# Optimization experiments

Hardware: AMD Instinct MI355X
Metric: run time of the kernel (lower is better)

## Reference

```python
import jax, jax.numpy as jnp
import numpy as np

B, T, V, EMB, H, SRC, NSRC = 128, 128, 50000, 1024, 512, 100, 3
D = EMB + 2 * H + SRC          # 2148, actual concat dim (cim* executable path)
HALF = D // 2                  # 1074
NUM_LABELS = 2


def setup_inputs() -> dict:
    key = jax.random.key(0)
    ks = jax.random.split(key, 32)
    s = 0.05
    n = lambda k, shp: jax.random.normal(k, shp, dtype=jnp.float32) * s
    inp = {
        "article": jax.random.randint(ks[0], (B, T), 0, V),
        "positions": jax.random.randint(ks[1], (B,), 0, T),
        "srcs": jax.random.randint(ks[2], (B,), 0, NSRC),
        "E": jax.random.normal(ks[3], (V, EMB), dtype=jnp.float32),
        "src_emb": n(ks[4], (NSRC, SRC)),
        # BiLSTM layer 0 (input EMB), forward / backward direction cells
        "Wih0f": n(ks[5], (4 * H, EMB)), "Whh0f": n(ks[6], (4 * H, H)),
        "bih0f": n(ks[7], (4 * H,)),     "bhh0f": n(ks[8], (4 * H,)),
        "Wih0b": n(ks[9], (4 * H, EMB)), "Whh0b": n(ks[10], (4 * H, H)),
        "bih0b": n(ks[11], (4 * H,)),    "bhh0b": n(ks[12], (4 * H,)),
        # BiLSTM layer 1 (input 2H)
        "Wih1f": n(ks[13], (4 * H, 2 * H)), "Whh1f": n(ks[14], (4 * H, H)),
        "bih1f": n(ks[15], (4 * H,)),       "bhh1f": n(ks[16], (4 * H,)),
        "Wih1b": n(ks[17], (4 * H, 2 * H)), "Whh1b": n(ks[18], (4 * H, H)),
        "bih1b": n(ks[19], (4 * H,)),       "bhh1b": n(ks[20], (4 * H,)),
        "dW": n(ks[21], (HALF, D)), "db": n(ks[22], (HALF,)),
        "cW": n(ks[23], (NUM_LABELS, HALF)), "cb": n(ks[24], (NUM_LABELS,)),
    }
    return inp


def _cell(x, h, c, Wih, Whh, bih, bhh):
    # PyTorch LSTMCell math, gate order i, f, g, o
    g = x @ Wih.T + h @ Whh.T + (bih + bhh)
    i, f, gg, o = jnp.split(g, 4, axis=-1)
    c2 = jax.nn.sigmoid(f) * c + jax.nn.sigmoid(i) * jnp.tanh(gg)
    h2 = jax.nn.sigmoid(o) * jnp.tanh(c2)
    return h2, c2


def reference(article, positions, srcs, E, src_emb,
              Wih0f, Whh0f, bih0f, bhh0f, Wih0b, Whh0b, bih0b, bhh0b,
              Wih1f, Whh1f, bih1f, bhh1f, Wih1b, Whh1b, bih1b, bhh1b,
              dW, db, cW, cb):
    batch = article.shape[0]

    def step(carry, tok):
        (h1f, c1f, h1b, c1b, h2f, c2f, h2b, c2b) = carry
        x = E[tok]                                   # [B, EMB], one token per item per step
        h1f, c1f = _cell(x, h1f, c1f, Wih0f, Whh0f, bih0f, bhh0f)
        h1b, c1b = _cell(x, h1b, c1b, Wih0b, Whh0b, bih0b, bhh0b)
        x2 = jnp.concatenate([h1f, h1b], axis=-1)    # [B, 2H]
        h2f, c2f = _cell(x2, h2f, c2f, Wih1f, Whh1f, bih1f, bhh1f)
        h2b, c2b = _cell(x2, h2b, c2b, Wih1b, Whh1b, bih1b, bhh1b)
        return (h1f, c1f, h1b, c1b, h2f, c2f, h2b, c2b), None

    z = jnp.zeros((batch, H), dtype=jnp.float32)
    carry0 = (z, z, z, z, z, z, z, z)
    carry, _ = jax.lax.scan(step, carry0, article.T)  # scan over T timesteps
    context = jnp.concatenate([carry[4], carry[6]], axis=-1)  # last step encoded [B, 2H]

    target = E[article[jnp.arange(batch), positions]]  # [B, EMB]
    src_e = src_emb[srcs]                              # [B, SRC]

    rep = jnp.concatenate([target, context, src_e], axis=-1)  # [B, D]
    feat = jnp.tanh(rep @ dW.T + db)                   # dropout is identity in eval
    logits = feat @ cW.T + cb
    probs = jax.nn.sigmoid(logits)
    return logits, probs, target
```

## Files before the change

### kernel.cpp

```cpp
#include <hip/hip_runtime.h>
#include <hip/hip_bf16.h>

typedef short short8 __attribute__((ext_vector_type(8)));
typedef float float4v __attribute__((ext_vector_type(4)));
typedef __hip_bfloat16 b16;
typedef unsigned short ushort_t;

#define T_ 128

__device__ __forceinline__ float sigm(float x) { return 1.0f / (1.0f + __expf(-x)); }
__device__ __forceinline__ float blo(unsigned u) { return __uint_as_float(u << 16); }
__device__ __forceinline__ float bhi(unsigned u) { return __uint_as_float(u & 0xffff0000u); }
__device__ __forceinline__ unsigned pack2bf(float a, float b) {
  b16 ha = __float2bfloat16(a), hb = __float2bfloat16(b);
  return (unsigned)*(ushort_t*)&ha | ((unsigned)*(ushort_t*)&hb << 16);
}

__device__ __forceinline__ void load_lds16(const void* g, void* l) {
  __builtin_amdgcn_global_load_lds((const __attribute__((address_space(1))) void*)g,
                                   (__attribute__((address_space(3))) void*)l, 16, 0, 0);
}

__global__ void gather_x(const int* __restrict__ article, const float* __restrict__ E,
                         b16* __restrict__ Xg) {
  int r = blockIdx.x;
  int b = r & 127, t = r >> 7;
  int tok = article[b * T_ + t];
  const float4* src = (const float4*)(E + (size_t)tok * 1024);
  float4 v = src[threadIdx.x];
  b16* dst = Xg + (size_t)r * 1024 + threadIdx.x * 4;
  dst[0] = __float2bfloat16(v.x);
  dst[1] = __float2bfloat16(v.y);
  dst[2] = __float2bfloat16(v.z);
  dst[3] = __float2bfloat16(v.w);
}

__global__ void cvt_cat2(const float* __restrict__ s0, const float* __restrict__ s1,
                         b16* __restrict__ out, int rows_each, int k, int total) {
  for (int idx = blockIdx.x * 256 + threadIdx.x; idx < total; idx += gridDim.x * 256) {
    int row = idx / k, col = idx - row * k;
    float v = (row < rows_each) ? s0[(size_t)row * k + col]
                                : s1[(size_t)(row - rows_each) * k + col];
    out[idx] = __float2bfloat16(v);
  }
}

__global__ void prep_bias(const float* bf1, const float* bf2, const float* bb1,
                          const float* bb2, float* out) {
  int j = blockIdx.x * 256 + threadIdx.x;
  int c = j >> 11, jj = j & 2047;
  out[j] = c ? (bb1[jj] + bb2[jj]) : (bf1[jj] + bf2[jj]);
}

__global__ void prep_dw(const float* __restrict__ dW, const float* __restrict__ db,
                        b16* __restrict__ dWpad, float* __restrict__ dbpad) {
  int idx = blockIdx.x * 256 + threadIdx.x;
  int r = idx / 2176, k = idx - r * 2176;
  float v = (r < 1074 && k < 2148) ? dW[(size_t)r * 2148 + k] : 0.0f;
  dWpad[idx] = __float2bfloat16(v);
  if (idx < 1152) dbpad[idx] = (idx < 1074) ? db[idx] : 0.0f;
}

__global__ __launch_bounds__(256) void gemm_bt(
    const b16* __restrict__ A, const b16* __restrict__ B2, b16* __restrict__ C,
    const float* __restrict__ bias, int M, int N, int K, int act) {
  __shared__ __align__(16) b16 As[128 * 64];
  __shared__ __align__(16) b16 Bs[128 * 64];
  const int tid = threadIdx.x;
  const int w = tid >> 6, lane = tid & 63;
  const int quad = lane >> 4, lane16 = lane & 15;
  const int m0 = blockIdx.y * 128, n0 = blockIdx.x * 128;
  const int wm = (w >> 1) * 64, wn = (w & 1) * 64;
  float4v acc[4][4] = {};
  for (int kt = 0; kt < K; kt += 64) {
    __syncthreads();
    #pragma unroll
    for (int i = 0; i < 4; ++i) {
      int s = (i * 4 + w) * 64 + lane;
      int rr = s >> 3, ch = s & 7;
      int gch = ch ^ (rr & 7);
      load_lds16(A + (size_t)(m0 + rr) * K + kt + gch * 8, (char*)As + (i * 4 + w) * 1024);
      load_lds16(B2 + (size_t)(n0 + rr) * K + kt + gch * 8, (char*)Bs + (i * 4 + w) * 1024);
    }
    __syncthreads();
    #pragma unroll
    for (int ks = 0; ks < 2; ++ks) {
      short8 af[4], bfr[4];
      #pragma unroll
      for (int a = 0; a < 4; ++a) {
        int rr = wm + a * 16 + lane16;
        int gg = ks * 4 + quad;
        af[a] = *(const short8*)(As + rr * 64 + (gg ^ (rr & 7)) * 8);
      }
      #pragma unroll
      for (int b = 0; b < 4; ++b) {
        int rr = wn + b * 16 + lane16;
        int gg = ks * 4 + quad;
        bfr[b] = *(const short8*)(Bs + rr * 64 + (gg ^ (rr & 7)) * 8);
      }
      #pragma unroll
      for (int a = 0; a < 4; ++a)
        #pragma unroll
        for (int b = 0; b < 4; ++b)
          acc[a][b] = __builtin_amdgcn_mfma_f32_16x16x32_bf16(af[a], bfr[b], acc[a][b], 0, 0, 0);
    }
  }
  #pragma unroll
  for (int a = 0; a < 4; ++a) {
    #pragma unroll
    for (int b = 0; b < 4; ++b) {
      int col = n0 + wn + b * 16 + lane16;
      float bv = bias ? bias[col] : 0.0f;
      #pragma unroll
      for (int rg = 0; rg < 4; ++rg) {
        int row = m0 + wm + a * 16 + quad * 4 + rg;
        float v = acc[a][b][rg] + bv;
        if (act) v = tanhf(v);
        C[(size_t)row * N + col] = __float2bfloat16(v);
      }
    }
  }
}

__global__ __launch_bounds__(512) void lstm_scan(
    const b16* __restrict__ Xproj,
    const b16* __restrict__ Whh,
    b16* __restrict__ hseq,
    int* __restrict__ flags) {
  __shared__ __align__(16) b16 As[16 * 528];
  __shared__ __align__(16) float gbuf[8][16][16];
  const int tid = threadIdx.x;
  const int bid = blockIdx.x;
  const int p = bid >> 4, d = bid & 15;
  const int c = d >> 3, r = d & 7;
  const int rb = r * 16, hs = p * 32;
  const int w = tid >> 6, lane = tid & 63;
  const int quad = lane >> 4, lane16 = lane & 15;
  const int gate = w >> 1, half = w & 1;
  const int colbase = gate * 512 + hs + half * 16;

  short8 bfrag[16];
  {
    const b16* wp = Whh + ((size_t)(c * 2048 + colbase + lane16)) * 512 + quad * 8;
    #pragma unroll
    for (int ks = 0; ks < 16; ++ks) bfrag[ks] = *(const short8*)(wp + ks * 32);
  }
  const int bloc = tid >> 4, hp = tid & 15;
  float cs0 = 0.0f, cs1 = 0.0f;

  for (int t = 0; t < T_; ++t) {
    unsigned xpr[4];
    if (tid < 256) {
      const unsigned* xb =
          (const unsigned*)(Xproj + ((size_t)t * 128 + rb + bloc) * 4096 + c * 2048 + hs + hp * 2);
      #pragma unroll
      for (int g4 = 0; g4 < 4; ++g4) xpr[g4] = xb[g4 * 256];
    }
    float4v acc = {0.f, 0.f, 0.f, 0.f};
    if (t > 0) {
      if (tid == 0) {
        int* fp = flags + ((t - 1) * 16 + d) * 16;
        while (__hip_atomic_load(fp, __ATOMIC_RELAXED, __HIP_MEMORY_SCOPE_AGENT) < 16) {}
      }
      __syncthreads();
      {
        const int row = tid >> 5, chunk = tid & 31;
        const b16* g = hseq + ((size_t)(t - 1) * 128 + rb + row) * 1024 + c * 512 + chunk * 16;
        uint4 v0, v1;
        asm volatile("global_load_dwordx4 %0, %2, off sc0 sc1\n\t"
                     "global_load_dwordx4 %1, %2, off offset:16 sc0 sc1"
                     : "=&v"(v0), "=&v"(v1) : "v"(g) : "memory");
        asm volatile("s_waitcnt vmcnt(0)" ::: "memory");
        *(uint4*)(As + row * 528 + chunk * 16) = v0;
        *(uint4*)(As + row * 528 + chunk * 16 + 8) = v1;
      }
      __syncthreads();
      #pragma unroll
      for (int ks = 0; ks < 16; ++ks) {
        short8 af = *(const short8*)(As + lane16 * 528 + ks * 32 + quad * 8);
        acc = __builtin_amdgcn_mfma_f32_16x16x32_bf16(af, bfrag[ks], acc, 0, 0, 0);
      }
    }
    #pragma unroll
    for (int rg = 0; rg < 4; ++rg) gbuf[w][quad * 4 + rg][lane16] = acc[rg];
    __syncthreads();
    if (tid < 256) {
      const size_t xrow = (size_t)t * 128 + rb + bloc;
      const int hhalf = hp >> 3;
      const int ci = 2 * (hp & 7);
      float g0[4], g1[4];
      #pragma unroll
      for (int g4 = 0; g4 < 4; ++g4) {
        float2 gv = *(const float2*)&gbuf[g4 * 2 + hhalf][bloc][ci];
        g0[g4] = gv.x + blo(xpr[g4]);
        g1[g4] = gv.y + bhi(xpr[g4]);
      }
      float i0 = sigm(g0[0]), f0 = sigm(g0[1]), gg0 = tanhf(g0[2]), o0 = sigm(g0[3]);
      float i1 = sigm(g1[0]), f1 = sigm(g1[1]), gg1 = tanhf(g1[2]), o1 = sigm(g1[3]);
      cs0 = f0 * cs0 + i0 * gg0;
      cs1 = f1 * cs1 + i1 * gg1;
      unsigned hv = pack2bf(o0 * tanhf(cs0), o1 * tanhf(cs1));
      unsigned* ha = (unsigned*)(hseq + xrow * 1024 + c * 512 + hs) + hp;
      asm volatile("global_store_dword %0, %1, off sc0 sc1" :: "v"(ha), "v"(hv) : "memory");
    }
    asm volatile("s_waitcnt vmcnt(0)" ::: "memory");
    __syncthreads();
    if (tid == 0)
      __hip_atomic_fetch_add(&flags[(t * 16 + d) * 16], 1, __ATOMIC_RELAXED,
                             __HIP_MEMORY_SCOPE_AGENT);
  }
}

__global__ void build_rep(const int* __restrict__ article, const int* __restrict__ positions,
                          const int* __restrict__ srcs, const float* __restrict__ E,
                          const float* __restrict__ src_emb, const b16* __restrict__ Xg,
                          const b16* __restrict__ h2seq, b16* __restrict__ rep,
                          float* __restrict__ out) {
  int b = blockIdx.x, tid = threadIdx.x;
  int pos = positions[b], sc = srcs[b];
  for (int k = tid; k < 2176; k += 256) {
    b16 v;
    if (k < 1024)      v = Xg[((size_t)pos * 128 + b) * 1024 + k];
    else if (k < 2048) v = h2seq[((size_t)127 * 128 + b) * 1024 + (k - 1024)];
    else if (k < 2148) v = __float2bfloat16(src_emb[sc * 100 + (k - 2048)]);
    else               v = __float2bfloat16(0.0f);
    rep[(size_t)b * 2176 + k] = v;
  }
  int tok = article[b * T_ + pos];
  for (int k = tid; k < 1024; k += 256)
    out[512 + b * 1024 + k] = E[(size_t)tok * 1024 + k];
}

__global__ void classifier(const b16* __restrict__ feat, const float* __restrict__ cW,
                           const float* __restrict__ cb, float* __restrict__ out) {
  __shared__ float red[256];
  int tid = threadIdx.x;
  int pairIdx = tid >> 3, jc = tid & 7;
  int bl = pairIdx >> 1, l = pairIdx & 1;
  int b = blockIdx.x * 16 + bl;
  int j0 = jc * 135, j1 = (j0 + 135 < 1074) ? j0 + 135 : 1074;
  float s = 0.f;
  for (int j = j0; j < j1; ++j)
    s += __bfloat162float(feat[(size_t)b * 1152 + j]) * cW[l * 1074 + j];
  red[tid] = s;
  __syncthreads();
  if (jc == 0) {
    float tot = 0.f;
    #pragma unroll
    for (int q = 0; q < 8; ++q) tot += red[pairIdx * 8 + q];
    tot += cb[l];
    out[b * 2 + l] = tot;
    out[256 + b * 2 + l] = 1.0f / (1.0f + __expf(-tot));
  }
}

extern "C" void kernel_launch(void* const* d_in, const int* in_sizes, int n_in,
                              void* d_out, int out_size, void* d_ws, size_t ws_size,
                              hipStream_t stream) {
  const int* article = (const int*)d_in[0];
  const int* positions = (const int*)d_in[1];
  const int* srcs = (const int*)d_in[2];
  const float* E = (const float*)d_in[3];
  const float* src_emb = (const float*)d_in[4];
  const float* Wih0f = (const float*)d_in[5];
  const float* Whh0f = (const float*)d_in[6];
  const float* bih0f = (const float*)d_in[7];
  const float* bhh0f = (const float*)d_in[8];
  const float* Wih0b = (const float*)d_in[9];
  const float* Whh0b = (const float*)d_in[10];
  const float* bih0b = (const float*)d_in[11];
  const float* bhh0b = (const float*)d_in[12];
  const float* Wih1f = (const float*)d_in[13];
  const float* Whh1f = (const float*)d_in[14];
  const float* bih1f = (const float*)d_in[15];
  const float* bhh1f = (const float*)d_in[16];
  const float* Wih1b = (const float*)d_in[17];
  const float* Whh1b = (const float*)d_in[18];
  const float* bih1b = (const float*)d_in[19];
  const float* bhh1b = (const float*)d_in[20];
  const float* dW = (const float*)d_in[21];
  const float* db = (const float*)d_in[22];
  const float* cW = (const float*)d_in[23];
  const float* cb = (const float*)d_in[24];

  char* ws = (char*)d_ws;
  size_t off = 0;
  auto carve = [&](size_t bytes) -> void* {
    void* p = ws + off;
    off += (bytes + 255) & ~(size_t)255;
    return p;
  };
  b16* Xg    = (b16*)carve((size_t)16384 * 1024 * 2);
  b16* h1seq = (b16*)carve((size_t)16384 * 1024 * 2);
  b16* h2seq = (b16*)carve((size_t)16384 * 1024 * 2);
  b16* Xproj = (b16*)carve((size_t)16384 * 4096 * 2);
  b16* W0cat = (b16*)carve((size_t)4096 * 1024 * 2);
  b16* W1cat = (b16*)carve((size_t)4096 * 1024 * 2);
  b16* Whh0  = (b16*)carve((size_t)2 * 2048 * 512 * 2);
  b16* Whh1  = (b16*)carve((size_t)2 * 2048 * 512 * 2);
  b16* dWpad = (b16*)carve((size_t)1152 * 2176 * 2);
  b16* rep   = (b16*)carve((size_t)128 * 2176 * 2);
  b16* feat  = (b16*)carve((size_t)128 * 1152 * 2);
  float* bias0 = (float*)carve(4096 * 4);
  float* bias1 = (float*)carve(4096 * 4);
  float* dbpad = (float*)carve(1152 * 4);
  int* flags1 = (int*)carve(128 * 16 * 16 * 4);
  int* flags2 = (int*)carve(128 * 16 * 16 * 4);
  (void)ws_size; (void)in_sizes; (void)n_in; (void)out_size;

  hipMemsetAsync(flags1, 0, 2 * 128 * 16 * 16 * 4, stream);

  gather_x<<<16384, 256, 0, stream>>>(article, E, Xg);
  cvt_cat2<<<8192, 256, 0, stream>>>(Wih0f, Wih0b, W0cat, 2048, 1024, 4096 * 1024);
  cvt_cat2<<<8192, 256, 0, stream>>>(Wih1f, Wih1b, W1cat, 2048, 1024, 4096 * 1024);
  cvt_cat2<<<8192, 256, 0, stream>>>(Whh0f, Whh0b, Whh0, 2048, 512, 4096 * 512);
  cvt_cat2<<<8192, 256, 0, stream>>>(Whh1f, Whh1b, Whh1, 2048, 512, 4096 * 512);
  prep_bias<<<16, 256, 0, stream>>>(bih0f, bhh0f, bih0b, bhh0b, bias0);
  prep_bias<<<16, 256, 0, stream>>>(bih1f, bhh1f, bih1b, bhh1b, bias1);
  prep_dw<<<9792, 256, 0, stream>>>(dW, db, dWpad, dbpad);

  gemm_bt<<<dim3(32, 128), 256, 0, stream>>>(Xg, W0cat, Xproj, bias0, 16384, 4096, 1024, 0);
  lstm_scan<<<256, 512, 0, stream>>>(Xproj, Whh0, h1seq, flags1);
  gemm_bt<<<dim3(32, 128), 256, 0, stream>>>(h1seq, W1cat, Xproj, bias1, 16384, 4096, 1024, 0);
  lstm_scan<<<256, 512, 0, stream>>>(Xproj, Whh1, h2seq, flags2);

  build_rep<<<128, 256, 0, stream>>>(article, positions, srcs, E, src_emb, Xg, h2seq, rep,
                                     (float*)d_out);
  gemm_bt<<<dim3(9, 1), 256, 0, stream>>>(rep, dWpad, feat, dbpad, 128, 1152, 2176, 1);
  classifier<<<8, 256, 0, stream>>>(feat, cW, cb, (float*)d_out);
}
```

Baseline: 1.368 ms.

## Replace flag counters with sentinel-polled hidden-state data in LSTM scan

Removes the per-step atomic flag counters and block barriers in the persistent LSTM scan. The hidden-state buffers are now pre-filled with a 0xFFFF sentinel, and each thread polls its own 32-byte chunk of the previous step's h until no sentinel word remains. This drops the tid-0 spin, an extra __syncthreads, the store drain and the atomic add from every timestep. In exchange it adds two large memsets per call and depends on a real bf16 pair never encoding as 0xFFFFFFFF (a NaN pattern), which tanh outputs cannot produce.

```diff
diff --git a/kernel.cpp b/kernel.cpp
--- a/kernel.cpp
+++ b/kernel.cpp
@@ -125,8 +125,7 @@
 __global__ __launch_bounds__(512) void lstm_scan(
     const b16* __restrict__ Xproj,
     const b16* __restrict__ Whh,
-    b16* __restrict__ hseq,
-    int* __restrict__ flags) {
+    b16* __restrict__ hseq) {
   __shared__ __align__(16) b16 As[16 * 528];
   __shared__ __align__(16) float gbuf[8][16][16];
   const int tid = threadIdx.x;
@@ -146,6 +145,7 @@
     for (int ks = 0; ks < 16; ++ks) bfrag[ks] = *(const short8*)(wp + ks * 32);
   }
   const int bloc = tid >> 4, hp = tid & 15;
+  const int srow = tid >> 5, schunk = tid & 31;
   float cs0 = 0.0f, cs1 = 0.0f;
 
   for (int t = 0; t < T_; ++t) {
@@ -158,22 +158,28 @@
     }
     float4v acc = {0.f, 0.f, 0.f, 0.f};
     if (t > 0) {
-      if (tid == 0) {
-        int* fp = flags + ((t - 1) * 16 + d) * 16;
-        while (__hip_atomic_load(fp, __ATOMIC_RELAXED, __HIP_MEMORY_SCOPE_AGENT) < 16) {}
-      }
-      __syncthreads();
-      {
-        const int row = tid >> 5, chunk = tid & 31;
-        const b16* g = hseq + ((size_t)(t - 1) * 128 + rb + row) * 1024 + c * 512 + chunk * 16;
-        uint4 v0, v1;
-        asm volatile("global_load_dwordx4 %0, %2, off sc0 sc1\n\t"
-                     "global_load_dwordx4 %1, %2, off offset:16 sc0 sc1"
-                     : "=&v"(v0), "=&v"(v1) : "v"(g) : "memory");
+      const b16* g = hseq + ((size_t)(t - 1) * 128 + rb + srow) * 1024 + c * 512 + schunk * 16;
+      uint4 v0, v1;
+      int ok0 = 0, ok1 = 0;
+      while (true) {
+        if (!ok0)
+          asm volatile("global_load_dwordx4 %0, %1, off sc0 sc1"
+                       : "=v"(v0) : "v"(g) : "memory");
+        if (!ok1)
+          asm volatile("global_load_dwordx4 %0, %1, off offset:16 sc0 sc1"
+                       : "=v"(v1) : "v"(g) : "memory");
         asm volatile("s_waitcnt vmcnt(0)" ::: "memory");
-        *(uint4*)(As + row * 528 + chunk * 16) = v0;
-        *(uint4*)(As + row * 528 + chunk * 16 + 8) = v1;
-      }
+        if (!ok0)
+          ok0 = (v0.x != 0xFFFFFFFFu) & (v0.y != 0xFFFFFFFFu) &
+                (v0.z != 0xFFFFFFFFu) & (v0.w != 0xFFFFFFFFu);
+        if (!ok1)
+          ok1 = (v1.x != 0xFFFFFFFFu) & (v1.y != 0xFFFFFFFFu) &
+                (v1.z != 0xFFFFFFFFu) & (v1.w != 0xFFFFFFFFu);
+        if (__all(ok0 & ok1)) break;
+        __builtin_amdgcn_s_sleep(2);
+      }
+      *(uint4*)(As + srow * 528 + schunk * 16) = v0;
+      *(uint4*)(As + srow * 528 + schunk * 16 + 8) = v1;
       __syncthreads();
       #pragma unroll
       for (int ks = 0; ks < 16; ++ks) {
@@ -203,11 +209,6 @@
       unsigned* ha = (unsigned*)(hseq + xrow * 1024 + c * 512 + hs) + hp;
       asm volatile("global_store_dword %0, %1, off sc0 sc1" :: "v"(ha), "v"(hv) : "memory");
     }
-    asm volatile("s_waitcnt vmcnt(0)" ::: "memory");
-    __syncthreads();
-    if (tid == 0)
-      __hip_atomic_fetch_add(&flags[(t * 16 + d) * 16], 1, __ATOMIC_RELAXED,
-                             __HIP_MEMORY_SCOPE_AGENT);
   }
 }
 
@@ -304,11 +305,10 @@
   float* bias0 = (float*)carve(4096 * 4);
   float* bias1 = (float*)carve(4096 * 4);
   float* dbpad = (float*)carve(1152 * 4);
-  int* flags1 = (int*)carve(128 * 16 * 16 * 4);
-  int* flags2 = (int*)carve(128 * 16 * 16 * 4);
   (void)ws_size; (void)in_sizes; (void)n_in; (void)out_size;
 
-  hipMemsetAsync(flags1, 0, 2 * 128 * 16 * 16 * 4, stream);
+  hipMemsetAsync(h1seq, 0xFF, (size_t)16384 * 1024 * 2, stream);
+  hipMemsetAsync(h2seq, 0xFF, (size_t)16384 * 1024 * 2, stream);
 
   gather_x<<<16384, 256, 0, stream>>>(article, E, Xg);
   cvt_cat2<<<8192, 256, 0, stream>>>(Wih0f, Wih0b, W0cat, 2048, 1024, 4096 * 1024);
@@ -320,9 +320,9 @@
   prep_dw<<<9792, 256, 0, stream>>>(dW, db, dWpad, dbpad);
 
   gemm_bt<<<dim3(32, 128), 256, 0, stream>>>(Xg, W0cat, Xproj, bias0, 16384, 4096, 1024, 0);
-  lstm_scan<<<256, 512, 0, stream>>>(Xproj, Whh0, h1seq, flags1);
+  lstm_scan<<<256, 512, 0, stream>>>(Xproj, Whh0, h1seq);
   gemm_bt<<<dim3(32, 128), 256, 0, stream>>>(h1seq, W1cat, Xproj, bias1, 16384, 4096, 1024, 0);
-  lstm_scan<<<256, 512, 0, stream>>>(Xproj, Whh1, h2seq, flags2);
+  lstm_scan<<<256, 512, 0, stream>>>(Xproj, Whh1, h2seq);
 
   build_rep<<<128, 256, 0, stream>>>(article, positions, srcs, E, src_emb, Xg, h2seq, rep,
                                      (float*)d_out);
```

Measured after the change: 1.633 ms. 1.19x slower.

## Replace counter-based step barrier with per-wave flags and split MFMA accumulators

Applied to the files above, without the earlier changes.

The cross-block step synchronisation in the LSTM scan changes from one thread spinning on an atomic counter followed by a block barrier to per-wave flag slots. Each producing wave writes its own flag once its h stores land, and each consuming thread polls only the flag covering the h chunk it loads. This removes two __syncthreads and the atomic add per step from the recurrence's critical path. The MFMA chain is also split into four independent accumulators to shorten the dependency chain. In exchange the flag array grows fourfold and many threads now poll global memory.

```diff
diff --git a/kernel.cpp b/kernel.cpp
--- a/kernel.cpp
+++ b/kernel.cpp
@@ -146,6 +146,7 @@
     for (int ks = 0; ks < 16; ++ks) bfrag[ks] = *(const short8*)(wp + ks * 32);
   }
   const int bloc = tid >> 4, hp = tid & 15;
+  const int srow = tid >> 5, schunk = tid & 31;
   float cs0 = 0.0f, cs1 = 0.0f;
 
   for (int t = 0; t < T_; ++t) {
@@ -156,33 +157,40 @@
       #pragma unroll
       for (int g4 = 0; g4 < 4; ++g4) xpr[g4] = xb[g4 * 256];
     }
-    float4v acc = {0.f, 0.f, 0.f, 0.f};
+    float4v acc0 = {0.f, 0.f, 0.f, 0.f}, acc1 = {0.f, 0.f, 0.f, 0.f};
+    float4v acc2 = {0.f, 0.f, 0.f, 0.f}, acc3 = {0.f, 0.f, 0.f, 0.f};
     if (t > 0) {
-      if (tid == 0) {
-        int* fp = flags + ((t - 1) * 16 + d) * 16;
-        while (__hip_atomic_load(fp, __ATOMIC_RELAXED, __HIP_MEMORY_SCOPE_AGENT) < 16) {}
-      }
+      const int* fp = flags + (((t - 1) * 16 + d) << 6) + (schunk >> 1) * 4 + (srow >> 2);
+      int fv;
+      do {
+        asm volatile("global_load_dword %0, %1, off sc0 sc1\n\t"
+                     "s_waitcnt vmcnt(0)"
+                     : "=v"(fv) : "v"(fp) : "memory");
+      } while (fv == 0);
+      const b16* g = hseq + ((size_t)(t - 1) * 128 + rb + srow) * 1024 + c * 512 + schunk * 16;
+      uint4 v0, v1;
+      asm volatile("global_load_dwordx4 %0, %2, off sc0 sc1\n\t"
+                   "global_load_dwordx4 %1, %2, off offset:16 sc0 sc1"
+                   : "=&v"(v0), "=&v"(v1) : "v"(g) : "memory");
+      asm volatile("s_waitcnt vmcnt(0)" ::: "memory");
+      *(uint4*)(As + srow * 528 + schunk * 16) = v0;
+      *(uint4*)(As + srow * 528 + schunk * 16 + 8) = v1;
       __syncthreads();
-      {
-        const int row = tid >> 5, chunk = tid & 31;
-        const b16* g = hseq + ((size_t)(t - 1) * 128 + rb + row) * 1024 + c * 512 + chunk * 16;
-        uint4 v0, v1;
-        asm volatile("global_load_dwordx4 %0, %2, off sc0 sc1\n\t"
-                     "global_load_dwordx4 %1, %2, off offset:16 sc0 sc1"
-                     : "=&v"(v0), "=&v"(v1) : "v"(g) : "memory");
-        asm volatile("s_waitcnt vmcnt(0)" ::: "memory");
-        *(uint4*)(As + row * 528 + chunk * 16) = v0;
-        *(uint4*)(As + row * 528 + chunk * 16 + 8) = v1;
-      }
-      __syncthreads();
-      #pragma unroll
-      for (int ks = 0; ks < 16; ++ks) {
-        short8 af = *(const short8*)(As + lane16 * 528 + ks * 32 + quad * 8);
-        acc = __builtin_amdgcn_mfma_f32_16x16x32_bf16(af, bfrag[ks], acc, 0, 0, 0);
-      }
-    }
-    #pragma unroll
-    for (int rg = 0; rg < 4; ++rg) gbuf[w][quad * 4 + rg][lane16] = acc[rg];
+      #pragma unroll
+      for (int ks = 0; ks < 16; ks += 4) {
+        short8 a0 = *(const short8*)(As + lane16 * 528 + (ks + 0) * 32 + quad * 8);
+        short8 a1 = *(const short8*)(As + lane16 * 528 + (ks + 1) * 32 + quad * 8);
+        short8 a2 = *(const short8*)(As + lane16 * 528 + (ks + 2) * 32 + quad * 8);
+        short8 a3 = *(const short8*)(As + lane16 * 528 + (ks + 3) * 32 + quad * 8);
+        acc0 = __builtin_amdgcn_mfma_f32_16x16x32_bf16(a0, bfrag[ks + 0], acc0, 0, 0, 0);
+        acc1 = __builtin_amdgcn_mfma_f32_16x16x32_bf16(a1, bfrag[ks + 1], acc1, 0, 0, 0);
+        acc2 = __builtin_amdgcn_mfma_f32_16x16x32_bf16(a2, bfrag[ks + 2], acc2, 0, 0, 0);
+        acc3 = __builtin_amdgcn_mfma_f32_16x16x32_bf16(a3, bfrag[ks + 3], acc3, 0, 0, 0);
+      }
+    }
+    #pragma unroll
+    for (int rg = 0; rg < 4; ++rg)
+      gbuf[w][quad * 4 + rg][lane16] = acc0[rg] + acc1[rg] + acc2[rg] + acc3[rg];
     __syncthreads();
     if (tid < 256) {
       const size_t xrow = (size_t)t * 128 + rb + bloc;
@@ -202,12 +210,13 @@
       unsigned hv = pack2bf(o0 * tanhf(cs0), o1 * tanhf(cs1));
       unsigned* ha = (unsigned*)(hseq + xrow * 1024 + c * 512 + hs) + hp;
       asm volatile("global_store_dword %0, %1, off sc0 sc1" :: "v"(ha), "v"(hv) : "memory");
-    }
-    asm volatile("s_waitcnt vmcnt(0)" ::: "memory");
-    __syncthreads();
-    if (tid == 0)
-      __hip_atomic_fetch_add(&flags[(t * 16 + d) * 16], 1, __ATOMIC_RELAXED,
-                             __HIP_MEMORY_SCOPE_AGENT);
+      asm volatile("s_waitcnt vmcnt(0)" ::: "memory");
+      if (lane == 0) {
+        int one = 1;
+        const int* fq = flags + ((t * 16 + d) << 6) + p * 4 + w;
+        asm volatile("global_store_dword %0, %1, off sc0 sc1" :: "v"(fq), "v"(one) : "memory");
+      }
+    }
   }
 }
 
@@ -304,11 +313,11 @@
   float* bias0 = (float*)carve(4096 * 4);
   float* bias1 = (float*)carve(4096 * 4);
   float* dbpad = (float*)carve(1152 * 4);
-  int* flags1 = (int*)carve(128 * 16 * 16 * 4);
-  int* flags2 = (int*)carve(128 * 16 * 16 * 4);
+  int* flags1 = (int*)carve(128 * 16 * 64 * 4);
+  int* flags2 = (int*)carve(128 * 16 * 64 * 4);
   (void)ws_size; (void)in_sizes; (void)n_in; (void)out_size;
 
-  hipMemsetAsync(flags1, 0, 2 * 128 * 16 * 16 * 4, stream);
+  hipMemsetAsync(flags1, 0, 2 * 128 * 16 * 64 * 4, stream);
 
   gather_x<<<16384, 256, 0, stream>>>(article, E, Xg);
   cvt_cat2<<<8192, 256, 0, stream>>>(Wih0f, Wih0b, W0cat, 2048, 1024, 4096 * 1024);
```

Result: slower. 2.603 ms (+90.3%).

## Fuse LSTM input projection into persistent recurrent scan kernel

Applied to the files above, without the earlier changes.

Removes the separate large input-projection GEMMs and the Xproj buffer. Each scan block now keeps its slice of the input weight matrix in registers and computes x@Wih per timestep, staging x rows into LDS with global_load_lds, then adds the recurrent product and bias before the cell update. This removes the write and read of a 16384x4096 bf16 intermediate and two GEMM launches. In exchange it adds input-projection MFMA work to every step of the serial scan and raises register pressure with 48 short8 fragments per lane.

```diff
diff --git a/kernel.cpp b/kernel.cpp
--- a/kernel.cpp
+++ b/kernel.cpp
@@ -9,8 +9,6 @@
 #define T_ 128
 
 __device__ __forceinline__ float sigm(float x) { return 1.0f / (1.0f + __expf(-x)); }
-__device__ __forceinline__ float blo(unsigned u) { return __uint_as_float(u << 16); }
-__device__ __forceinline__ float bhi(unsigned u) { return __uint_as_float(u & 0xffff0000u); }
 __device__ __forceinline__ unsigned pack2bf(float a, float b) {
   b16 ha = __float2bfloat16(a), hb = __float2bfloat16(b);
   return (unsigned)*(ushort_t*)&ha | ((unsigned)*(ushort_t*)&hb << 16);
@@ -122,12 +120,15 @@
   }
 }
 
-__global__ __launch_bounds__(512) void lstm_scan(
-    const b16* __restrict__ Xproj,
+__global__ __launch_bounds__(512, 2) void lstm_scan_f(
+    const b16* __restrict__ xin,
+    const b16* __restrict__ Wcat,
     const b16* __restrict__ Whh,
-    b16* __restrict__ hseq,
+    const float* __restrict__ bias,
+    b16* __restrict__ hout,
     int* __restrict__ flags) {
-  __shared__ __align__(16) b16 As[16 * 528];
+  __shared__ __align__(16) b16 Xs[16 * 1032];
+  __shared__ __align__(16) b16 Hs[16 * 528];
   __shared__ __align__(16) float gbuf[8][16][16];
   const int tid = threadIdx.x;
   const int bid = blockIdx.x;
@@ -139,50 +140,72 @@
   const int gate = w >> 1, half = w & 1;
   const int colbase = gate * 512 + hs + half * 16;
 
-  short8 bfrag[16];
+  short8 bin[32];
+  {
+    const b16* wp = Wcat + ((size_t)(c * 2048 + colbase + lane16)) * 1024 + quad * 8;
+    #pragma unroll
+    for (int ks = 0; ks < 32; ++ks) bin[ks] = *(const short8*)(wp + ks * 32);
+  }
+  short8 bhh[16];
   {
     const b16* wp = Whh + ((size_t)(c * 2048 + colbase + lane16)) * 512 + quad * 8;
     #pragma unroll
-    for (int ks = 0; ks < 16; ++ks) bfrag[ks] = *(const short8*)(wp + ks * 32);
+    for (int ks = 0; ks < 16; ++ks) bhh[ks] = *(const short8*)(wp + ks * 32);
   }
   const int bloc = tid >> 4, hp = tid & 15;
+  const int srow = tid >> 5, schunk = tid & 31;
+  float bs0[4], bs1[4];
+  #pragma unroll
+  for (int g4 = 0; g4 < 4; ++g4) {
+    bs0[g4] = bias[c * 2048 + g4 * 512 + hs + 2 * hp];
+    bs1[g4] = bias[c * 2048 + g4 * 512 + hs + 2 * hp + 1];
+  }
   float cs0 = 0.0f, cs1 = 0.0f;
 
   for (int t = 0; t < T_; ++t) {
-    unsigned xpr[4];
-    if (tid < 256) {
-      const unsigned* xb =
-          (const unsigned*)(Xproj + ((size_t)t * 128 + rb + bloc) * 4096 + c * 2048 + hs + hp * 2);
-      #pragma unroll
-      for (int g4 = 0; g4 < 4; ++g4) xpr[g4] = xb[g4 * 256];
-    }
-    float4v acc = {0.f, 0.f, 0.f, 0.f};
+    if (t > 0 && tid == 0) {
+      const int* fp = flags + ((t - 1) * 16 + d) * 16;
+      while (__hip_atomic_load(fp, __ATOMIC_RELAXED, __HIP_MEMORY_SCOPE_AGENT) < 16) {}
+    }
+    if (t > 0) __syncthreads();
+    #pragma unroll
+    for (int i = 0; i < 4; ++i) {
+      int idx = i * 8 + w;
+      int row = idx >> 1, hrow = idx & 1;
+      load_lds16(xin + ((size_t)t * 128 + rb + row) * 1024 + hrow * 512 + lane * 8,
+                 (char*)Xs + row * 2064 + hrow * 1024);
+    }
     if (t > 0) {
-      if (tid == 0) {
-        int* fp = flags + ((t - 1) * 16 + d) * 16;
-        while (__hip_atomic_load(fp, __ATOMIC_RELAXED, __HIP_MEMORY_SCOPE_AGENT) < 16) {}
-      }
-      __syncthreads();
-      {
-        const int row = tid >> 5, chunk = tid & 31;
-        const b16* g = hseq + ((size_t)(t - 1) * 128 + rb + row) * 1024 + c * 512 + chunk * 16;
-        uint4 v0, v1;
-        asm volatile("global_load_dwordx4 %0, %2, off sc0 sc1\n\t"
-                     "global_load_dwordx4 %1, %2, off offset:16 sc0 sc1"
-                     : "=&v"(v0), "=&v"(v1) : "v"(g) : "memory");
-        asm volatile("s_waitcnt vmcnt(0)" ::: "memory");
-        *(uint4*)(As + row * 528 + chunk * 16) = v0;
-        *(uint4*)(As + row * 528 + chunk * 16 + 8) = v1;
-      }
-      __syncthreads();
-      #pragma unroll
-      for (int ks = 0; ks < 16; ++ks) {
-        short8 af = *(const short8*)(As + lane16 * 528 + ks * 32 + quad * 8);
-        acc = __builtin_amdgcn_mfma_f32_16x16x32_bf16(af, bfrag[ks], acc, 0, 0, 0);
-      }
-    }
-    #pragma unroll
-    for (int rg = 0; rg < 4; ++rg) gbuf[w][quad * 4 + rg][lane16] = acc[rg];
+      const b16* g = hout + ((size_t)(t - 1) * 128 + rb + srow) * 1024 + c * 512 + schunk * 16;
+      uint4 v0, v1;
+      asm volatile("global_load_dwordx4 %0, %2, off sc0 sc1\n\t"
+                   "global_load_dwordx4 %1, %2, off offset:16 sc0 sc1"
+                   : "=&v"(v0), "=&v"(v1) : "v"(g) : "memory");
+      asm volatile("s_waitcnt vmcnt(0)" ::: "memory");
+      *(uint4*)(Hs + srow * 528 + schunk * 16) = v0;
+      *(uint4*)(Hs + srow * 528 + schunk * 16 + 8) = v1;
+    }
+    __syncthreads();
+    float4v acc0 = {0.f, 0.f, 0.f, 0.f}, acc1 = {0.f, 0.f, 0.f, 0.f};
+    #pragma unroll
+    for (int ks = 0; ks < 32; ks += 2) {
+      short8 a0 = *(const short8*)(Xs + lane16 * 1032 + ks * 32 + quad * 8);
+      short8 a1 = *(const short8*)(Xs + lane16 * 1032 + (ks + 1) * 32 + quad * 8);
+      acc0 = __builtin_amdgcn_mfma_f32_16x16x32_bf16(a0, bin[ks], acc0, 0, 0, 0);
+      acc1 = __builtin_amdgcn_mfma_f32_16x16x32_bf16(a1, bin[ks + 1], acc1, 0, 0, 0);
+    }
+    if (t > 0) {
+      #pragma unroll
+      for (int ks = 0; ks < 16; ks += 2) {
+        short8 a0 = *(const short8*)(Hs + lane16 * 528 + ks * 32 + quad * 8);
+        short8 a1 = *(const short8*)(Hs + lane16 * 528 + (ks + 1) * 32 + quad * 8);
+        acc0 = __builtin_amdgcn_mfma_f32_16x16x32_bf16(a0, bhh[ks], acc0, 0, 0, 0);
+        acc1 = __builtin_amdgcn_mfma_f32_16x16x32_bf16(a1, bhh[ks + 1], acc1, 0, 0, 0);
+      }
+    }
+    #pragma unroll
+    for (int rg = 0; rg < 4; ++rg)
+      gbuf[w][quad * 4 + rg][lane16] = acc0[rg] + acc1[rg];
     __syncthreads();
     if (tid < 256) {
       const size_t xrow = (size_t)t * 128 + rb + bloc;
@@ -192,15 +215,15 @@
       #pragma unroll
       for (int g4 = 0; g4 < 4; ++g4) {
         float2 gv = *(const float2*)&gbuf[g4 * 2 + hhalf][bloc][ci];
-        g0[g4] = gv.x + blo(xpr[g4]);
-        g1[g4] = gv.y + bhi(xpr[g4]);
+        g0[g4] = gv.x + bs0[g4];
+        g1[g4] = gv.y + bs1[g4];
       }
       float i0 = sigm(g0[0]), f0 = sigm(g0[1]), gg0 = tanhf(g0[2]), o0 = sigm(g0[3]);
       float i1 = sigm(g1[0]), f1 = sigm(g1[1]), gg1 = tanhf(g1[2]), o1 = sigm(g1[3]);
       cs0 = f0 * cs0 + i0 * gg0;
       cs1 = f1 * cs1 + i1 * gg1;
       unsigned hv = pack2bf(o0 * tanhf(cs0), o1 * tanhf(cs1));
-      unsigned* ha = (unsigned*)(hseq + xrow * 1024 + c * 512 + hs) + hp;
+      unsigned* ha = (unsigned*)(hout + xrow * 1024 + c * 512 + hs) + hp;
       asm volatile("global_store_dword %0, %1, off sc0 sc1" :: "v"(ha), "v"(hv) : "memory");
     }
     asm volatile("s_waitcnt vmcnt(0)" ::: "memory");
@@ -293,7 +316,6 @@
   b16* Xg    = (b16*)carve((size_t)16384 * 1024 * 2);
   b16* h1seq = (b16*)carve((size_t)16384 * 1024 * 2);
   b16* h2seq = (b16*)carve((size_t)16384 * 1024 * 2);
-  b16* Xproj = (b16*)carve((size_t)16384 * 4096 * 2);
   b16* W0cat = (b16*)carve((size_t)4096 * 1024 * 2);
   b16* W1cat = (b16*)carve((size_t)4096 * 1024 * 2);
   b16* Whh0  = (b16*)carve((size_t)2 * 2048 * 512 * 2);
@@ -319,10 +341,8 @@
   prep_bias<<<16, 256, 0, stream>>>(bih1f, bhh1f, bih1b, bhh1b, bias1);
   prep_dw<<<9792, 256, 0, stream>>>(dW, db, dWpad, dbpad);
 
-  gemm_bt<<<dim3(32, 128), 256, 0, stream>>>(Xg, W0cat, Xproj, bias0, 16384, 4096, 1024, 0);
-  lstm_scan<<<256, 512, 0, stream>>>(Xproj, Whh0, h1seq, flags1);
-  gemm_bt<<<dim3(32, 128), 256, 0, stream>>>(h1seq, W1cat, Xproj, bias1, 16384, 4096, 1024, 0);
-  lstm_scan<<<256, 512, 0, stream>>>(Xproj, Whh1, h2seq, flags2);
+  lstm_scan_f<<<256, 512, 0, stream>>>(Xg, W0cat, Whh0, bias0, h1seq, flags1);
+  lstm_scan_f<<<256, 512, 0, stream>>>(h1seq, W1cat, Whh1, bias1, h2seq, flags2);
 
   build_rep<<<128, 256, 0, stream>>>(article, positions, srcs, E, src_emb, Xg, h2seq, rep,
                                      (float*)d_out);
```

Result: no change. 1.384 ms (+1.2%).
